# Kernel optimization log

Measured on AMD Instinct MI355X. Metric: run time of the kernel, lower is better.

## Reference

```python
import jax, jax.numpy as jnp
import numpy as np

HEADS = 4
DIM_HEAD = 32
SCALE = DIM_HEAD ** -0.5
EPS = 1e-5


def setup_inputs() -> dict:
    key = jax.random.key(0)
    ks = jax.random.split(key, 4)
    B, C, H, W = 16, 128, 32, 32
    hid = HEADS * DIM_HEAD  # 128
    return {
        "x": jax.random.normal(ks[0], (B, C, H, W), jnp.float32),
        "gn_weight": jnp.ones((C,), jnp.float32),
        "gn_bias": jnp.zeros((C,), jnp.float32),
        "w_qkv": jax.random.normal(ks[1], (3 * hid, C), jnp.float32) * 0.05,  # 1x1 conv, no bias
        "w_out": jax.random.normal(ks[2], (C, hid), jnp.float32) * 0.05,      # 1x1 conv
        "b_out": jax.random.normal(ks[3], (C,), jnp.float32) * 0.05,
    }


def reference(x, gn_weight, gn_bias, w_qkv, w_out, b_out):
    B, C, H, W = x.shape
    N = H * W
    # GroupNorm(num_groups=1): normalize over (C, H, W) per sample, per-channel affine
    mu = x.mean(axis=(1, 2, 3), keepdims=True)
    var = x.var(axis=(1, 2, 3), keepdims=True)
    xn = (x - mu) * jax.lax.rsqrt(var + EPS)
    xn = xn * gn_weight[None, :, None, None] + gn_bias[None, :, None, None]

    xf = xn.reshape(B, C, N)  # b c n
    qkv = jnp.einsum('bcn,oc->bon', xf, w_qkv)  # 1x1 conv == matmul over channels
    q, k, v = jnp.split(qkv, 3, axis=1)

    def to_heads(t):  # 'b (h c) x y -> b h (x y) c'
        return t.reshape(B, HEADS, DIM_HEAD, N).transpose(0, 1, 3, 2)  # b h n c

    q, k, v = map(to_heads, (q, k, v))

    q = jax.nn.softmax(q, axis=-2) * SCALE  # softmax over spatial tokens
    k = jax.nn.softmax(k, axis=-1)          # softmax over channel dim

    # Faithful to source einsums: contract over CHANNEL dim -> (b, h, N, N) context
    context = jnp.einsum('bhdc,bhec->bhde', k, v)      # b h n n
    out = jnp.einsum('bhde,bhdc->bhec', context, q)    # b h n c

    # 'b h (x y) c -> b (h c) x y'
    outf = out.transpose(0, 1, 3, 2).reshape(B, HEADS * DIM_HEAD, N)
    y = jnp.einsum('bcn,oc->bon', outf, w_out) + b_out[None, :, None]
    return y.reshape(B, C, H, W)
```

## Files before the change

### kernel.cpp

```cpp
#include <hip/hip_runtime.h>
#include <math.h>

#define CIN 128
#define NTOK 1024
#define SCALE_Q 0.17677669529663687f
#define GN_EPS 1e-5f
#define PB (CIN * NTOK)

#define WS_WQKVB 0
#define WS_WVT   16384
#define WS_PSTATS 24576
#define WS_PQSUM 25088
#define WS_PMT   57856
#define WS_WEFF  1106432
#define WS_BIAS  1237504

typedef __bf16 bf16x8 __attribute__((ext_vector_type(8)));
typedef float f32x4 __attribute__((ext_vector_type(4)));

__device__ __forceinline__ unsigned short f2bf(float f) {
    union { float f; unsigned u; } v; v.f = f;
    unsigned r = v.u + 0x7fffu + ((v.u >> 16) & 1u);
    return (unsigned short)(r >> 16);
}
__device__ __forceinline__ unsigned pack2(float a, float b) {
    return (unsigned)f2bf(a) | ((unsigned)f2bf(b) << 16);
}

__global__ __launch_bounds__(256) void k_pre(const float* __restrict__ x,
                                             const float* __restrict__ wqkv,
                                             float* __restrict__ ws) {
    float* pstats = ws + WS_PSTATS;
    unsigned short* wqkvb = (unsigned short*)(ws + WS_WQKVB);
    unsigned short* wvT = (unsigned short*)(ws + WS_WVT);
    __shared__ float sD[8];
    int bid = blockIdx.x, t = threadIdx.x;
    int lane = t & 63, wave = t >> 6;
    const float4* p = (const float4*)(x + (size_t)bid * 8192);
    float s = 0.f, s2 = 0.f;
    #pragma unroll
    for (int i = 0; i < 8; i++) {
        float4 v = p[t + 256 * i];
        s += v.x + v.y + v.z + v.w;
        s2 += v.x * v.x + v.y * v.y + v.z * v.z + v.w * v.w;
    }
    #pragma unroll
    for (int off = 32; off; off >>= 1) {
        s += __shfl_down(s, off);
        s2 += __shfl_down(s2, off);
    }
    if (lane == 0) { sD[wave * 2] = s; sD[wave * 2 + 1] = s2; }
    if (bid < 32) {
        float4 v = ((const float4*)(wqkv + bid * 1024))[t];
        uint2 pk2; pk2.x = pack2(v.x, v.y); pk2.y = pack2(v.z, v.w);
        *(uint2*)(wqkvb + bid * 1024 + t * 4) = pk2;
    } else if (bid < 48) {
        int g = bid - 32;
        int kk = g * 8 + (t >> 5), cq = t & 31;
        float v0 = wqkv[(256 + cq * 4 + 0) * 128 + kk];
        float v1 = wqkv[(256 + cq * 4 + 1) * 128 + kk];
        float v2 = wqkv[(256 + cq * 4 + 2) * 128 + kk];
        float v3 = wqkv[(256 + cq * 4 + 3) * 128 + kk];
        uint2 pk2; pk2.x = pack2(v0, v1); pk2.y = pack2(v2, v3);
        *(uint2*)(wvT + kk * 128 + cq * 4) = pk2;
    }
    __syncthreads();
    if (t == 0) {
        pstats[bid * 2] = sD[0] + sD[2] + sD[4] + sD[6];
        pstats[bid * 2 + 1] = sD[1] + sD[3] + sD[5] + sD[7];
    }
}

__global__ __launch_bounds__(512, 1) void k_qk(const float* __restrict__ x,
                                               const float* __restrict__ gw,
                                               const float* __restrict__ gb,
                                               float* __restrict__ ws) {
    __shared__ __align__(16) char smem[122880];
    unsigned short (*Al)[136] = (unsigned short(*)[136])smem;
    float (*Xl)[68] = (float(*)[68])(smem + 17408);
    unsigned short (*kTl)[68] = (unsigned short(*)[68])(smem + 17408);
    unsigned short (*qTl)[68] = (unsigned short(*)[68])(smem + 34816);
    unsigned short (*Bl)[136] = (unsigned short(*)[136])(smem + 52224);
    float* sD = (float*)(smem + 121856);

    unsigned short* wqkvb = (unsigned short*)(ws + WS_WQKVB);
    float* pstats = ws + WS_PSTATS;
    float* pqsum = ws + WS_PQSUM;
    float* pMT = ws + WS_PMT;

    int bid = blockIdx.x, t = threadIdx.x;
    int b = bid >> 4, nt = bid & 15;
    int lane = t & 63, wave = t >> 6;
    int l15 = lane & 15, lk = (lane >> 4) * 8;
    int sel = wave >> 1;
    int wn0 = (wave & 1) * 32;

    if (t < 32) sD[t] = pstats[b * 32 + t];
    int cx = t >> 2, qtr = t & 3;
    const float4* xsrc = (const float4*)(x + ((size_t)b * CIN + cx) * NTOK + nt * 64 + qtr * 16);
    float4 xr0 = xsrc[0], xr1 = xsrc[1], xr2 = xsrc[2], xr3 = xsrc[3];
    {
        int row = t >> 1, hf = t & 1;
        const uint4* src = (const uint4*)(wqkvb + (size_t)row * CIN + hf * 64);
        uint4* dst = (uint4*)&Bl[row][hf * 64];
        #pragma unroll
        for (int j = 0; j < 8; j++) dst[j] = src[j];
    }
    __syncthreads();
    float mu, rsv;
    {
        float s = 0.f, s2 = 0.f;
        #pragma unroll
        for (int i = 0; i < 16; i++) { s += sD[2 * i]; s2 += sD[2 * i + 1]; }
        mu = s * (1.f / PB);
        float var = s2 * (1.f / PB) - mu * mu;
        rsv = rsqrtf(var + GN_EPS);
    }
    {
        float g = gw[cx] * rsv, bb = gb[cx] - mu * g;
        float4 r0 = { xr0.x * g + bb, xr0.y * g + bb, xr0.z * g + bb, xr0.w * g + bb };
        float4 r1 = { xr1.x * g + bb, xr1.y * g + bb, xr1.z * g + bb, xr1.w * g + bb };
        float4 r2 = { xr2.x * g + bb, xr2.y * g + bb, xr2.z * g + bb, xr2.w * g + bb };
        float4 r3 = { xr3.x * g + bb, xr3.y * g + bb, xr3.z * g + bb, xr3.w * g + bb };
        *(float4*)&Xl[cx][qtr * 16 + 0] = r0;
        *(float4*)&Xl[cx][qtr * 16 + 4] = r1;
        *(float4*)&Xl[cx][qtr * 16 + 8] = r2;
        *(float4*)&Xl[cx][qtr * 16 + 12] = r3;
    }
    __syncthreads();
    {
        int n = t & 63, kq = (t >> 6) * 16;
        unsigned pk[8];
        #pragma unroll
        for (int j = 0; j < 8; j++) pk[j] = pack2(Xl[kq + 2 * j][n], Xl[kq + 2 * j + 1][n]);
        *(uint4*)&Al[n][kq] = *(uint4*)pk;
        *(uint4*)(&Al[n][kq] + 8) = *(uint4*)(pk + 4);
    }
    __syncthreads();
    f32x4 acc[2][4] = {};
    #pragma unroll
    for (int ks = 0; ks < 4; ks++) {
        bf16x8 av[2], bv[4];
        #pragma unroll
        for (int i = 0; i < 2; i++) av[i] = *(const bf16x8*)&Al[wn0 + i * 16 + l15][ks * 32 + lk];
        #pragma unroll
        for (int j = 0; j < 4; j++) bv[j] = *(const bf16x8*)&Bl[sel * 64 + j * 16 + l15][ks * 32 + lk];
        #pragma unroll
        for (int i = 0; i < 2; i++)
            #pragma unroll
            for (int j = 0; j < 4; j++)
                acc[i][j] = __builtin_amdgcn_mfma_f32_16x16x32_bf16(av[i], bv[j], acc[i][j], 0, 0, 0);
    }
    float e[2][4][4];
    #pragma unroll
    for (int i = 0; i < 2; i++)
        #pragma unroll
        for (int j = 0; j < 4; j++)
            #pragma unroll
            for (int r = 0; r < 4; r++) e[i][j][r] = __expf(acc[i][j][r]);

    if (sel >= 2) {
        #pragma unroll
        for (int i = 0; i < 2; i++)
            #pragma unroll
            for (int r = 0; r < 4; r++) {
                float e01 = e[i][0][r] + e[i][1][r];
                float e23 = e[i][2][r] + e[i][3][r];
                #pragma unroll
                for (int m = 1; m < 16; m <<= 1) {
                    e01 += __shfl_xor(e01, m);
                    e23 += __shfl_xor(e23, m);
                }
                float i01 = 1.f / e01, i23 = 1.f / e23;
                e[i][0][r] *= i01; e[i][1][r] *= i01;
                e[i][2][r] *= i23; e[i][3][r] *= i23;
            }
        #pragma unroll
        for (int i = 0; i < 2; i++)
            #pragma unroll
            for (int j = 0; j < 4; j++) {
                int ch = (sel - 2) * 64 + j * 16 + l15;
                int tokb = wn0 + i * 16 + (lane >> 4) * 4;
                *(unsigned*)&kTl[ch][tokb] = pack2(e[i][j][0], e[i][j][1]);
                *(unsigned*)&kTl[ch][tokb + 2] = pack2(e[i][j][2], e[i][j][3]);
            }
    } else {
        #pragma unroll
        for (int i = 0; i < 2; i++)
            #pragma unroll
            for (int j = 0; j < 4; j++) {
                int ch = sel * 64 + j * 16 + l15;
                int tokb = wn0 + i * 16 + (lane >> 4) * 4;
                *(unsigned*)&qTl[ch][tokb] = pack2(e[i][j][0], e[i][j][1]);
                *(unsigned*)&qTl[ch][tokb + 2] = pack2(e[i][j][2], e[i][j][3]);
            }
        #pragma unroll
        for (int j = 0; j < 4; j++) {
            float sq = 0.f;
            #pragma unroll
            for (int i = 0; i < 2; i++)
                #pragma unroll
                for (int r = 0; r < 4; r++) sq += e[i][j][r];
            sq += __shfl_xor(sq, 16);
            sq += __shfl_xor(sq, 32);
            if (lane < 16) sD[(wave & 1) * 128 + sel * 64 + j * 16 + lane] = sq;
        }
    }
    __syncthreads();
    if (t < 128) pqsum[(size_t)bid * 128 + t] = sD[t] + sD[128 + t];
    if (wave < 4) {
        int h = wave;
        f32x4 mac[2][2] = {};
        #pragma unroll
        for (int ks = 0; ks < 2; ks++) {
            bf16x8 av[2], bv[2];
            #pragma unroll
            for (int i = 0; i < 2; i++) av[i] = *(const bf16x8*)&qTl[h * 32 + i * 16 + l15][ks * 32 + lk];
            #pragma unroll
            for (int j = 0; j < 2; j++) bv[j] = *(const bf16x8*)&kTl[h * 32 + j * 16 + l15][ks * 32 + lk];
            #pragma unroll
            for (int i = 0; i < 2; i++)
                #pragma unroll
                for (int j = 0; j < 2; j++)
                    mac[i][j] = __builtin_amdgcn_mfma_f32_16x16x32_bf16(av[i], bv[j], mac[i][j], 0, 0, 0);
        }
        float* pmb = pMT + ((size_t)bid * 4 + h) * 1024;
        #pragma unroll
        for (int i = 0; i < 2; i++)
            #pragma unroll
            for (int j = 0; j < 2; j++)
                #pragma unroll
                for (int r = 0; r < 4; r++)
                    pmb[(i * 16 + (lane >> 4) * 4 + r) * 32 + j * 16 + l15] = mac[i][j][r];
    }
}

__global__ __launch_bounds__(512, 1) void k_weff(const float* __restrict__ gw,
                                                 const float* __restrict__ gb,
                                                 const float* __restrict__ wout,
                                                 const float* __restrict__ bout,
                                                 float* __restrict__ ws) {
    __shared__ __align__(16) char smem[116736];
    unsigned short (*pMTb)[32][40] = (unsigned short(*)[32][40])smem;
    unsigned short (*wvTb)[136] = (unsigned short(*)[136])(smem + 10240);
    unsigned short (*WeffL)[136] = (unsigned short(*)[136])(smem + 10240);
    unsigned short (*woutb)[136] = (unsigned short(*)[136])(smem + 45056);
    unsigned short (*B2T)[136] = (unsigned short(*)[136])(smem + 79872);
    float* sD = (float*)(smem + 114688);

    float* pstats = ws + WS_PSTATS;
    float* pqsum = ws + WS_PQSUM;
    float* pMT = ws + WS_PMT;
    unsigned short* wvT = (unsigned short*)(ws + WS_WVT);
    unsigned short* weffg = (unsigned short*)(ws + WS_WEFF);
    float* biasg = ws + WS_BIAS;

    int b = blockIdx.x, t = threadIdx.x;
    int lane = t & 63, wave = t >> 6;
    int l15 = lane & 15, lk = (lane >> 4) * 8;

    if (t < 32) sD[384 + t] = pstats[b * 32 + t];
    if (t < 128) {
        float s = 0.f;
        #pragma unroll
        for (int i = 0; i < 16; i++) s += pqsum[(size_t)(b * 16 + i) * 128 + t];
        sD[t] = SCALE_Q / s;
    }
    #pragma unroll
    for (int s2 = 0; s2 < 2; s2++) {
        int f4 = t * 2 + s2;
        int h = f4 >> 8, c = (f4 >> 3) & 31, cp0 = (f4 & 7) * 4;
        float4 m = { 0.f, 0.f, 0.f, 0.f };
        for (int i = 0; i < 16; i++) {
            float4 v = *(const float4*)&pMT[(((size_t)(b * 16 + i)) * 4 + h) * 1024 + c * 32 + cp0];
            m.x += v.x; m.y += v.y; m.z += v.z; m.w += v.w;
        }
        uint2 u; u.x = pack2(m.x, m.y); u.y = pack2(m.z, m.w);
        *(uint2*)&pMTb[h][c][cp0] = u;
    }
    {
        int row = t >> 2, q4 = t & 3;
        const uint4* src = (const uint4*)(wvT + row * 128) + q4 * 4;
        #pragma unroll
        for (int m = 0; m < 4; m++) *(uint4*)&wvTb[row][q4 * 32 + m * 8] = src[m];
    }
    {
        int row = t >> 2, q4 = t & 3;
        const float4* src = (const float4*)(wout + row * 128 + q4 * 32);
        #pragma unroll
        for (int i = 0; i < 8; i++) {
            float4 v = src[i];
            uint2 u; u.x = pack2(v.x, v.y); u.y = pack2(v.z, v.w);
            *(uint2*)&woutb[row][q4 * 32 + i * 4] = u;
        }
    }
    __syncthreads();
    if (t < 128) {
        float s = 0.f, s2 = 0.f;
        #pragma unroll
        for (int i = 0; i < 16; i++) { s += sD[384 + 2 * i]; s2 += sD[384 + 2 * i + 1]; }
        float mu = s * (1.f / PB);
        float var = s2 * (1.f / PB) - mu * mu;
        float rs = rsqrtf(var + GN_EPS);
        float gsc = gw[t] * rs;
        sD[128 + t] = gsc;
        sD[256 + t] = gb[t] - mu * gsc;
    }
    __syncthreads();
    {
        int h = wave >> 1, kh = wave & 1;
        f32x4 mac[2][4] = {};
        bf16x8 av[2];
        #pragma unroll
        for (int i = 0; i < 2; i++) av[i] = *(const bf16x8*)&pMTb[h][i * 16 + l15][lk];
        #pragma unroll
        for (int j = 0; j < 4; j++) {
            bf16x8 bv = *(const bf16x8*)&wvTb[kh * 64 + j * 16 + l15][h * 32 + lk];
            #pragma unroll
            for (int i = 0; i < 2; i++)
                mac[i][j] = __builtin_amdgcn_mfma_f32_16x16x32_bf16(av[i], bv, mac[i][j], 0, 0, 0);
        }
        #pragma unroll
        for (int i = 0; i < 2; i++)
            #pragma unroll
            for (int j = 0; j < 4; j++) {
                int k = kh * 64 + j * 16 + l15;
                int cb = h * 32 + i * 16 + (lane >> 4) * 4;
                float q0 = sD[cb], q1 = sD[cb + 1], q2 = sD[cb + 2], q3 = sD[cb + 3];
                uint2 u;
                u.x = pack2(mac[i][j][0] * q0, mac[i][j][1] * q1);
                u.y = pack2(mac[i][j][2] * q2, mac[i][j][3] * q3);
                *(uint2*)&B2T[k][cb] = u;
            }
    }
    __syncthreads();
    {
        f32x4 acc[8] = {};
        #pragma unroll
        for (int ks = 0; ks < 4; ks++) {
            bf16x8 av = *(const bf16x8*)&woutb[wave * 16 + l15][ks * 32 + lk];
            #pragma unroll
            for (int j = 0; j < 8; j++) {
                bf16x8 bv = *(const bf16x8*)&B2T[j * 16 + l15][ks * 32 + lk];
                acc[j] = __builtin_amdgcn_mfma_f32_16x16x32_bf16(av, bv, acc[j], 0, 0, 0);
            }
        }
        float gs[8], bbv[8];
        #pragma unroll
        for (int j = 0; j < 8; j++) {
            int k = j * 16 + l15;
            gs[j] = sD[128 + k];
            bbv[j] = sD[256 + k];
        }
        #pragma unroll
        for (int r = 0; r < 4; r++) {
            int o = wave * 16 + (lane >> 4) * 4 + r;
            float pb = 0.f;
            #pragma unroll
            for (int j = 0; j < 8; j++) {
                float wv = acc[j][r];
                pb += wv * bbv[j];
                WeffL[o][j * 16 + l15] = f2bf(wv * gs[j]);
            }
            pb += __shfl_xor(pb, 1);
            pb += __shfl_xor(pb, 2);
            pb += __shfl_xor(pb, 4);
            pb += __shfl_xor(pb, 8);
            if (l15 == 0) biasg[b * 128 + o] = bout[o] + pb;
        }
    }
    __syncthreads();
    {
        int row = t >> 2, q4 = t & 3;
        #pragma unroll
        for (int m = 0; m < 4; m++)
            *(uint4*)(weffg + (size_t)b * 16384 + row * 128 + q4 * 32 + m * 8) =
                *(uint4*)&WeffL[row][q4 * 32 + m * 8];
    }
}

__global__ __launch_bounds__(512, 1) void k_out2(const float* __restrict__ x,
                                                 float* __restrict__ ws,
                                                 float* __restrict__ y) {
    __shared__ __align__(16) char smem[87552];
    unsigned short (*Wfb)[136] = (unsigned short(*)[136])smem;
    float (*Xl)[68] = (float(*)[68])(smem + 34816);
    unsigned short (*xT)[136] = (unsigned short(*)[136])(smem + 69632);
    float* sDb = (float*)(smem + 87040);

    unsigned short* weffg = (unsigned short*)(ws + WS_WEFF);
    float* biasg = ws + WS_BIAS;

    int nt = blockIdx.x, b = blockIdx.y, t = threadIdx.x;
    int lane = t & 63, wave = t >> 6;
    int l15 = lane & 15, lk = (lane >> 4) * 8;

    if (t < 128) sDb[t] = biasg[b * 128 + t];
    {
        int row = t >> 2, q4 = t & 3;
        const uint4* src = (const uint4*)(weffg + (size_t)b * 16384 + row * 128) + q4 * 4;
        #pragma unroll
        for (int m = 0; m < 4; m++) *(uint4*)&Wfb[row][q4 * 32 + m * 8] = src[m];
    }
    {
        int cx = t >> 2, qtr = t & 3;
        const float4* xsrc = (const float4*)(x + ((size_t)b * CIN + cx) * NTOK + nt * 64 + qtr * 16);
        #pragma unroll
        for (int i = 0; i < 4; i++) *(float4*)&Xl[cx][qtr * 16 + i * 4] = xsrc[i];
    }
    __syncthreads();
    {
        int n = t & 63, kq = (t >> 6) * 16;
        unsigned pk[8];
        #pragma unroll
        for (int j = 0; j < 8; j++) pk[j] = pack2(Xl[kq + 2 * j][n], Xl[kq + 2 * j + 1][n]);
        *(uint4*)&xT[n][kq] = *(uint4*)pk;
        *(uint4*)(&xT[n][kq] + 8) = *(uint4*)(pk + 4);
    }
    __syncthreads();
    int o0 = (wave >> 1) * 32, n0 = (wave & 1) * 32;
    f32x4 acc[2][2] = {};
    #pragma unroll
    for (int ks = 0; ks < 4; ks++) {
        bf16x8 av[2], bv[2];
        #pragma unroll
        for (int i = 0; i < 2; i++) av[i] = *(const bf16x8*)&Wfb[o0 + i * 16 + l15][ks * 32 + lk];
        #pragma unroll
        for (int j = 0; j < 2; j++) bv[j] = *(const bf16x8*)&xT[n0 + j * 16 + l15][ks * 32 + lk];
        #pragma unroll
        for (int i = 0; i < 2; i++)
            #pragma unroll
            for (int j = 0; j < 2; j++)
                acc[i][j] = __builtin_amdgcn_mfma_f32_16x16x32_bf16(av[i], bv[j], acc[i][j], 0, 0, 0);
    }
    #pragma unroll
    for (int i = 0; i < 2; i++)
        #pragma unroll
        for (int r = 0; r < 4; r++) {
            int o = o0 + i * 16 + (lane >> 4) * 4 + r;
            float bias = sDb[o];
            float* yp = y + ((size_t)b * CIN + o) * NTOK + nt * 64 + n0;
            #pragma unroll
            for (int j = 0; j < 2; j++) yp[j * 16 + l15] = acc[i][j][r] + bias;
        }
}

extern "C" void kernel_launch(void* const* d_in, const int* in_sizes, int n_in,
                              void* d_out, int out_size, void* d_ws, size_t ws_size,
                              hipStream_t stream) {
    const float* x = (const float*)d_in[0];
    const float* gw = (const float*)d_in[1];
    const float* gb = (const float*)d_in[2];
    const float* wqkv = (const float*)d_in[3];
    const float* wout = (const float*)d_in[4];
    const float* bout = (const float*)d_in[5];
    float* y = (float*)d_out;
    float* ws = (float*)d_ws;

    k_pre<<<dim3(256), 256, 0, stream>>>(x, wqkv, ws);
    k_qk<<<dim3(256), 512, 0, stream>>>(x, gw, gb, ws);
    k_weff<<<dim3(16), 512, 0, stream>>>(gw, gb, wout, bout, ws);
    k_out2<<<dim3(16, 16), 512, 0, stream>>>(x, ws, y);
}
```

Baseline: 97.63 us.

## Fuse Weff fold into output kernel and reduce partials with atomics

```diff
diff --git a/kernel.cpp b/kernel.cpp
--- a/kernel.cpp
+++ b/kernel.cpp
@@ -10,10 +10,8 @@
 #define WS_WQKVB 0
 #define WS_WVT   16384
 #define WS_PSTATS 24576
-#define WS_PQSUM 25088
-#define WS_PMT   57856
-#define WS_WEFF  1106432
-#define WS_BIAS  1237504
+#define WS_QSUMG 25088
+#define WS_MG    27136
 
 typedef __bf16 bf16x8 __attribute__((ext_vector_type(8)));
 typedef float f32x4 __attribute__((ext_vector_type(4)));
@@ -36,6 +34,8 @@
     __shared__ float sD[8];
     int bid = blockIdx.x, t = threadIdx.x;
     int lane = t & 63, wave = t >> 6;
+    int gid = bid * 256 + t;
+    if (gid < 18432) ws[WS_QSUMG + gid] = 0.f;
     const float4* p = (const float4*)(x + (size_t)bid * 8192);
     float s = 0.f, s2 = 0.f;
     #pragma unroll
@@ -75,30 +75,35 @@
                                                const float* __restrict__ gw,
                                                const float* __restrict__ gb,
                                                float* __restrict__ ws) {
-    __shared__ __align__(16) char smem[122880];
+    __shared__ __align__(16) char smem[121856];
     unsigned short (*Al)[136] = (unsigned short(*)[136])smem;
-    float (*Xl)[68] = (float(*)[68])(smem + 17408);
-    unsigned short (*kTl)[68] = (unsigned short(*)[68])(smem + 17408);
-    unsigned short (*qTl)[68] = (unsigned short(*)[68])(smem + 34816);
-    unsigned short (*Bl)[136] = (unsigned short(*)[136])(smem + 52224);
-    float* sD = (float*)(smem + 121856);
+    unsigned short (*Bl)[136] = (unsigned short(*)[136])(smem + 17408);
+    unsigned short (*kTl)[68] = (unsigned short(*)[68])(smem + 87040);
+    unsigned short (*qTl)[68] = (unsigned short(*)[68])(smem + 104448);
 
     unsigned short* wqkvb = (unsigned short*)(ws + WS_WQKVB);
     float* pstats = ws + WS_PSTATS;
-    float* pqsum = ws + WS_PQSUM;
-    float* pMT = ws + WS_PMT;
+    float* qsumg = ws + WS_QSUMG;
+    float* Mg = ws + WS_MG;
 
     int bid = blockIdx.x, t = threadIdx.x;
     int b = bid >> 4, nt = bid & 15;
     int lane = t & 63, wave = t >> 6;
     int l15 = lane & 15, lk = (lane >> 4) * 8;
-    int sel = wave >> 1;
-    int wn0 = (wave & 1) * 32;
-
-    if (t < 32) sD[t] = pstats[b * 32 + t];
-    int cx = t >> 2, qtr = t & 3;
-    const float4* xsrc = (const float4*)(x + ((size_t)b * CIN + cx) * NTOK + nt * 64 + qtr * 16);
-    float4 xr0 = xsrc[0], xr1 = xsrc[1], xr2 = xsrc[2], xr3 = xsrc[3];
+    int sel = wave >> 1, wn0 = (wave & 1) * 32;
+
+    float mu, rsv;
+    {
+        float s = 0.f, s2 = 0.f;
+        #pragma unroll
+        for (int i = 0; i < 16; i++) {
+            s += pstats[b * 32 + 2 * i];
+            s2 += pstats[b * 32 + 2 * i + 1];
+        }
+        mu = s * (1.f / PB);
+        float var = s2 * (1.f / PB) - mu * mu;
+        rsv = rsqrtf(var + GN_EPS);
+    }
     {
         int row = t >> 1, hf = t & 1;
         const uint4* src = (const uint4*)(wqkvb + (size_t)row * CIN + hf * 64);
@@ -106,35 +111,19 @@
         #pragma unroll
         for (int j = 0; j < 8; j++) dst[j] = src[j];
     }
-    __syncthreads();
-    float mu, rsv;
-    {
-        float s = 0.f, s2 = 0.f;
-        #pragma unroll
-        for (int i = 0; i < 16; i++) { s += sD[2 * i]; s2 += sD[2 * i + 1]; }
-        mu = s * (1.f / PB);
-        float var = s2 * (1.f / PB) - mu * mu;
-        rsv = rsqrtf(var + GN_EPS);
-    }
-    {
-        float g = gw[cx] * rsv, bb = gb[cx] - mu * g;
-        float4 r0 = { xr0.x * g + bb, xr0.y * g + bb, xr0.z * g + bb, xr0.w * g + bb };
-        float4 r1 = { xr1.x * g + bb, xr1.y * g + bb, xr1.z * g + bb, xr1.w * g + bb };
-        float4 r2 = { xr2.x * g + bb, xr2.y * g + bb, xr2.z * g + bb, xr2.w * g + bb };
-        float4 r3 = { xr3.x * g + bb, xr3.y * g + bb, xr3.z * g + bb, xr3.w * g + bb };
-        *(float4*)&Xl[cx][qtr * 16 + 0] = r0;
-        *(float4*)&Xl[cx][qtr * 16 + 4] = r1;
-        *(float4*)&Xl[cx][qtr * 16 + 8] = r2;
-        *(float4*)&Xl[cx][qtr * 16 + 12] = r3;
-    }
-    __syncthreads();
-    {
-        int n = t & 63, kq = (t >> 6) * 16;
-        unsigned pk[8];
-        #pragma unroll
-        for (int j = 0; j < 8; j++) pk[j] = pack2(Xl[kq + 2 * j][n], Xl[kq + 2 * j + 1][n]);
-        *(uint4*)&Al[n][kq] = *(uint4*)pk;
-        *(uint4*)(&Al[n][kq] + 8) = *(uint4*)(pk + 4);
+    {
+        int c = t & 127, seg = t >> 7;
+        const float4* xsrc = (const float4*)(x + ((size_t)b * CIN + c) * NTOK + nt * 64 + seg * 16);
+        float g = gw[c] * rsv, bb = gb[c] - mu * g;
+        #pragma unroll
+        for (int q4 = 0; q4 < 4; q4++) {
+            float4 v = xsrc[q4];
+            int n = seg * 16 + q4 * 4;
+            Al[n + 0][c] = f2bf(v.x * g + bb);
+            Al[n + 1][c] = f2bf(v.y * g + bb);
+            Al[n + 2][c] = f2bf(v.z * g + bb);
+            Al[n + 3][c] = f2bf(v.w * g + bb);
+        }
     }
     __syncthreads();
     f32x4 acc[2][4] = {};
@@ -203,11 +192,10 @@
                 for (int r = 0; r < 4; r++) sq += e[i][j][r];
             sq += __shfl_xor(sq, 16);
             sq += __shfl_xor(sq, 32);
-            if (lane < 16) sD[(wave & 1) * 128 + sel * 64 + j * 16 + lane] = sq;
-        }
-    }
-    __syncthreads();
-    if (t < 128) pqsum[(size_t)bid * 128 + t] = sD[t] + sD[128 + t];
+            if (lane < 16) atomicAdd(&qsumg[b * 128 + sel * 64 + j * 16 + lane], sq);
+        }
+    }
+    __syncthreads();
     if (wave < 4) {
         int h = wave;
         f32x4 mac[2][2] = {};
@@ -224,63 +212,82 @@
                 for (int j = 0; j < 2; j++)
                     mac[i][j] = __builtin_amdgcn_mfma_f32_16x16x32_bf16(av[i], bv[j], mac[i][j], 0, 0, 0);
         }
-        float* pmb = pMT + ((size_t)bid * 4 + h) * 1024;
+        float* mb = Mg + (size_t)b * 4096 + h * 1024;
         #pragma unroll
         for (int i = 0; i < 2; i++)
             #pragma unroll
             for (int j = 0; j < 2; j++)
                 #pragma unroll
                 for (int r = 0; r < 4; r++)
-                    pmb[(i * 16 + (lane >> 4) * 4 + r) * 32 + j * 16 + l15] = mac[i][j][r];
-    }
-}
-
-__global__ __launch_bounds__(512, 1) void k_weff(const float* __restrict__ gw,
-                                                 const float* __restrict__ gb,
-                                                 const float* __restrict__ wout,
-                                                 const float* __restrict__ bout,
-                                                 float* __restrict__ ws) {
-    __shared__ __align__(16) char smem[116736];
-    unsigned short (*pMTb)[32][40] = (unsigned short(*)[32][40])smem;
-    unsigned short (*wvTb)[136] = (unsigned short(*)[136])(smem + 10240);
-    unsigned short (*WeffL)[136] = (unsigned short(*)[136])(smem + 10240);
-    unsigned short (*woutb)[136] = (unsigned short(*)[136])(smem + 45056);
-    unsigned short (*B2T)[136] = (unsigned short(*)[136])(smem + 79872);
-    float* sD = (float*)(smem + 114688);
+                    atomicAdd(&mb[(i * 16 + (lane >> 4) * 4 + r) * 32 + j * 16 + l15], mac[i][j][r]);
+    }
+}
+
+__global__ __launch_bounds__(512, 1) void k_fold_out(const float* __restrict__ x,
+                                                     const float* __restrict__ gw,
+                                                     const float* __restrict__ gb,
+                                                     const float* __restrict__ wout,
+                                                     const float* __restrict__ bout,
+                                                     float* __restrict__ ws,
+                                                     float* __restrict__ y) {
+    __shared__ __align__(16) char smem[132608];
+    unsigned short (*Al)[136] = (unsigned short(*)[136])smem;
+    unsigned short (*pMTb)[32][40] = (unsigned short(*)[32][40])(smem + 17408);
+    unsigned short (*wvTb)[136] = (unsigned short(*)[136])(smem + 27648);
+    unsigned short (*WeffL)[136] = (unsigned short(*)[136])(smem + 27648);
+    unsigned short (*woutb)[136] = (unsigned short(*)[136])(smem + 62464);
+    unsigned short (*B2T)[136] = (unsigned short(*)[136])(smem + 97280);
+    float* biasL = (float*)(smem + 132096);
 
     float* pstats = ws + WS_PSTATS;
-    float* pqsum = ws + WS_PQSUM;
-    float* pMT = ws + WS_PMT;
-    unsigned short* wvT = (unsigned short*)(ws + WS_WVT);
-    unsigned short* weffg = (unsigned short*)(ws + WS_WEFF);
-    float* biasg = ws + WS_BIAS;
-
-    int b = blockIdx.x, t = threadIdx.x;
+    float* qsumg = ws + WS_QSUMG;
+    float* Mg = ws + WS_MG;
+    unsigned short* wvTg = (unsigned short*)(ws + WS_WVT);
+
+    int bid = blockIdx.x, t = threadIdx.x;
+    int b = bid >> 4, nt = bid & 15;
     int lane = t & 63, wave = t >> 6;
     int l15 = lane & 15, lk = (lane >> 4) * 8;
 
-    if (t < 32) sD[384 + t] = pstats[b * 32 + t];
-    if (t < 128) {
-        float s = 0.f;
-        #pragma unroll
-        for (int i = 0; i < 16; i++) s += pqsum[(size_t)(b * 16 + i) * 128 + t];
-        sD[t] = SCALE_Q / s;
-    }
-    #pragma unroll
-    for (int s2 = 0; s2 < 2; s2++) {
-        int f4 = t * 2 + s2;
-        int h = f4 >> 8, c = (f4 >> 3) & 31, cp0 = (f4 & 7) * 4;
-        float4 m = { 0.f, 0.f, 0.f, 0.f };
+    float mu, rsv;
+    {
+        float s = 0.f, s2 = 0.f;
+        #pragma unroll
         for (int i = 0; i < 16; i++) {
-            float4 v = *(const float4*)&pMT[(((size_t)(b * 16 + i)) * 4 + h) * 1024 + c * 32 + cp0];
-            m.x += v.x; m.y += v.y; m.z += v.z; m.w += v.w;
-        }
-        uint2 u; u.x = pack2(m.x, m.y); u.y = pack2(m.z, m.w);
-        *(uint2*)&pMTb[h][c][cp0] = u;
+            s += pstats[b * 32 + 2 * i];
+            s2 += pstats[b * 32 + 2 * i + 1];
+        }
+        mu = s * (1.f / PB);
+        float var = s2 * (1.f / PB) - mu * mu;
+        rsv = rsqrtf(var + GN_EPS);
+    }
+    {
+        int c = t & 127, seg = t >> 7;
+        const float4* xsrc = (const float4*)(x + ((size_t)b * CIN + c) * NTOK + nt * 64 + seg * 16);
+        float g = gw[c] * rsv, bb = gb[c] - mu * g;
+        #pragma unroll
+        for (int q4 = 0; q4 < 4; q4++) {
+            float4 v = xsrc[q4];
+            int n = seg * 16 + q4 * 4;
+            Al[n + 0][c] = f2bf(v.x * g + bb);
+            Al[n + 1][c] = f2bf(v.y * g + bb);
+            Al[n + 2][c] = f2bf(v.z * g + bb);
+            Al[n + 3][c] = f2bf(v.w * g + bb);
+        }
+    }
+    {
+        int base = t * 8;
+        int h = base >> 10, idx = base & 1023, c = idx >> 5, cp0 = idx & 31;
+        float4 m0 = *(const float4*)&Mg[(size_t)b * 4096 + base];
+        float4 m1 = *(const float4*)&Mg[(size_t)b * 4096 + base + 4];
+        uint4 u;
+        u.x = pack2(m0.x, m0.y); u.y = pack2(m0.z, m0.w);
+        u.z = pack2(m1.x, m1.y); u.w = pack2(m1.z, m1.w);
+        *(uint4*)&pMTb[h][c][cp0] = u;
     }
     {
         int row = t >> 2, q4 = t & 3;
-        const uint4* src = (const uint4*)(wvT + row * 128) + q4 * 4;
+        const uint4* src = (const uint4*)(wvTg + row * 128) + q4 * 4;
         #pragma unroll
         for (int m = 0; m < 4; m++) *(uint4*)&wvTb[row][q4 * 32 + m * 8] = src[m];
     }
@@ -294,18 +301,7 @@
             *(uint2*)&woutb[row][q4 * 32 + i * 4] = u;
         }
     }
-    __syncthreads();
-    if (t < 128) {
-        float s = 0.f, s2 = 0.f;
-        #pragma unroll
-        for (int i = 0; i < 16; i++) { s += sD[384 + 2 * i]; s2 += sD[384 + 2 * i + 1]; }
-        float mu = s * (1.f / PB);
-        float var = s2 * (1.f / PB) - mu * mu;
-        float rs = rsqrtf(var + GN_EPS);
-        float gsc = gw[t] * rs;
-        sD[128 + t] = gsc;
-        sD[256 + t] = gb[t] - mu * gsc;
-    }
+    if (t < 128) biasL[t] = bout[t];
     __syncthreads();
     {
         int h = wave >> 1, kh = wave & 1;
@@ -321,128 +317,68 @@
                 mac[i][j] = __builtin_amdgcn_mfma_f32_16x16x32_bf16(av[i], bv, mac[i][j], 0, 0, 0);
         }
         #pragma unroll
-        for (int i = 0; i < 2; i++)
+        for (int i = 0; i < 2; i++) {
+            int cb = h * 32 + i * 16 + (lane >> 4) * 4;
+            float4 qs = *(const float4*)&qsumg[b * 128 + cb];
+            float q0 = SCALE_Q / qs.x, q1 = SCALE_Q / qs.y;
+            float q2 = SCALE_Q / qs.z, q3 = SCALE_Q / qs.w;
             #pragma unroll
             for (int j = 0; j < 4; j++) {
                 int k = kh * 64 + j * 16 + l15;
-                int cb = h * 32 + i * 16 + (lane >> 4) * 4;
-                float q0 = sD[cb], q1 = sD[cb + 1], q2 = sD[cb + 2], q3 = sD[cb + 3];
                 uint2 u;
                 u.x = pack2(mac[i][j][0] * q0, mac[i][j][1] * q1);
                 u.y = pack2(mac[i][j][2] * q2, mac[i][j][3] * q3);
                 *(uint2*)&B2T[k][cb] = u;
             }
-    }
-    __syncthreads();
-    {
-        f32x4 acc[8] = {};
+        }
+    }
+    __syncthreads();
+    {
+        f32x4 a2[8] = {};
         #pragma unroll
         for (int ks = 0; ks < 4; ks++) {
             bf16x8 av = *(const bf16x8*)&woutb[wave * 16 + l15][ks * 32 + lk];
             #pragma unroll
             for (int j = 0; j < 8; j++) {
                 bf16x8 bv = *(const bf16x8*)&B2T[j * 16 + l15][ks * 32 + lk];
-                acc[j] = __builtin_amdgcn_mfma_f32_16x16x32_bf16(av, bv, acc[j], 0, 0, 0);
-            }
-        }
-        float gs[8], bbv[8];
-        #pragma unroll
-        for (int j = 0; j < 8; j++) {
-            int k = j * 16 + l15;
-            gs[j] = sD[128 + k];
-            bbv[j] = sD[256 + k];
-        }
-        #pragma unroll
-        for (int r = 0; r < 4; r++) {
-            int o = wave * 16 + (lane >> 4) * 4 + r;
-            float pb = 0.f;
-            #pragma unroll
-            for (int j = 0; j < 8; j++) {
-                float wv = acc[j][r];
-                pb += wv * bbv[j];
-                WeffL[o][j * 16 + l15] = f2bf(wv * gs[j]);
-            }
-            pb += __shfl_xor(pb, 1);
-            pb += __shfl_xor(pb, 2);
-            pb += __shfl_xor(pb, 4);
-            pb += __shfl_xor(pb, 8);
-            if (l15 == 0) biasg[b * 128 + o] = bout[o] + pb;
-        }
-    }
-    __syncthreads();
-    {
-        int row = t >> 2, q4 = t & 3;
-        #pragma unroll
-        for (int m = 0; m < 4; m++)
-            *(uint4*)(weffg + (size_t)b * 16384 + row * 128 + q4 * 32 + m * 8) =
-                *(uint4*)&WeffL[row][q4 * 32 + m * 8];
-    }
-}
-
-__global__ __launch_bounds__(512, 1) void k_out2(const float* __restrict__ x,
-                                                 float* __restrict__ ws,
-                                                 float* __restrict__ y) {
-    __shared__ __align__(16) char smem[87552];
-    unsigned short (*Wfb)[136] = (unsigned short(*)[136])smem;
-    float (*Xl)[68] = (float(*)[68])(smem + 34816);
-    unsigned short (*xT)[136] = (unsigned short(*)[136])(smem + 69632);
-    float* sDb = (float*)(smem + 87040);
-
-    unsigned short* weffg = (unsigned short*)(ws + WS_WEFF);
-    float* biasg = ws + WS_BIAS;
-
-    int nt = blockIdx.x, b = blockIdx.y, t = threadIdx.x;
-    int lane = t & 63, wave = t >> 6;
-    int l15 = lane & 15, lk = (lane >> 4) * 8;
-
-    if (t < 128) sDb[t] = biasg[b * 128 + t];
-    {
-        int row = t >> 2, q4 = t & 3;
-        const uint4* src = (const uint4*)(weffg + (size_t)b * 16384 + row * 128) + q4 * 4;
-        #pragma unroll
-        for (int m = 0; m < 4; m++) *(uint4*)&Wfb[row][q4 * 32 + m * 8] = src[m];
-    }
-    {
-        int cx = t >> 2, qtr = t & 3;
-        const float4* xsrc = (const float4*)(x + ((size_t)b * CIN + cx) * NTOK + nt * 64 + qtr * 16);
-        #pragma unroll
-        for (int i = 0; i < 4; i++) *(float4*)&Xl[cx][qtr * 16 + i * 4] = xsrc[i];
-    }
-    __syncthreads();
-    {
-        int n = t & 63, kq = (t >> 6) * 16;
-        unsigned pk[8];
-        #pragma unroll
-        for (int j = 0; j < 8; j++) pk[j] = pack2(Xl[kq + 2 * j][n], Xl[kq + 2 * j + 1][n]);
-        *(uint4*)&xT[n][kq] = *(uint4*)pk;
-        *(uint4*)(&xT[n][kq] + 8) = *(uint4*)(pk + 4);
-    }
-    __syncthreads();
-    int o0 = (wave >> 1) * 32, n0 = (wave & 1) * 32;
-    f32x4 acc[2][2] = {};
-    #pragma unroll
-    for (int ks = 0; ks < 4; ks++) {
-        bf16x8 av[2], bv[2];
-        #pragma unroll
-        for (int i = 0; i < 2; i++) av[i] = *(const bf16x8*)&Wfb[o0 + i * 16 + l15][ks * 32 + lk];
-        #pragma unroll
-        for (int j = 0; j < 2; j++) bv[j] = *(const bf16x8*)&xT[n0 + j * 16 + l15][ks * 32 + lk];
-        #pragma unroll
-        for (int i = 0; i < 2; i++)
-            #pragma unroll
-            for (int j = 0; j < 2; j++)
-                acc[i][j] = __builtin_amdgcn_mfma_f32_16x16x32_bf16(av[i], bv[j], acc[i][j], 0, 0, 0);
-    }
-    #pragma unroll
-    for (int i = 0; i < 2; i++)
-        #pragma unroll
-        for (int r = 0; r < 4; r++) {
-            int o = o0 + i * 16 + (lane >> 4) * 4 + r;
-            float bias = sDb[o];
-            float* yp = y + ((size_t)b * CIN + o) * NTOK + nt * 64 + n0;
-            #pragma unroll
-            for (int j = 0; j < 2; j++) yp[j * 16 + l15] = acc[i][j][r] + bias;
-        }
+                a2[j] = __builtin_amdgcn_mfma_f32_16x16x32_bf16(av, bv, a2[j], 0, 0, 0);
+            }
+        }
+        __syncthreads();
+        #pragma unroll
+        for (int j = 0; j < 8; j++)
+            #pragma unroll
+            for (int r = 0; r < 4; r++)
+                WeffL[wave * 16 + (lane >> 4) * 4 + r][j * 16 + l15] = f2bf(a2[j][r]);
+    }
+    __syncthreads();
+    {
+        int o0 = (wave >> 1) * 32, n0 = (wave & 1) * 32;
+        f32x4 ya[2][2] = {};
+        #pragma unroll
+        for (int ks = 0; ks < 4; ks++) {
+            bf16x8 av[2], bv[2];
+            #pragma unroll
+            for (int i = 0; i < 2; i++) av[i] = *(const bf16x8*)&WeffL[o0 + i * 16 + l15][ks * 32 + lk];
+            #pragma unroll
+            for (int j = 0; j < 2; j++) bv[j] = *(const bf16x8*)&Al[n0 + j * 16 + l15][ks * 32 + lk];
+            #pragma unroll
+            for (int i = 0; i < 2; i++)
+                #pragma unroll
+                for (int j = 0; j < 2; j++)
+                    ya[i][j] = __builtin_amdgcn_mfma_f32_16x16x32_bf16(av[i], bv[j], ya[i][j], 0, 0, 0);
+        }
+        #pragma unroll
+        for (int i = 0; i < 2; i++)
+            #pragma unroll
+            for (int r = 0; r < 4; r++) {
+                int o = o0 + i * 16 + (lane >> 4) * 4 + r;
+                float bias = biasL[o];
+                float* yp = y + ((size_t)b * CIN + o) * NTOK + nt * 64 + n0;
+                #pragma unroll
+                for (int j = 0; j < 2; j++) yp[j * 16 + l15] = ya[i][j][r] + bias;
+            }
+    }
 }
 
 extern "C" void kernel_launch(void* const* d_in, const int* in_sizes, int n_in,
@@ -459,6 +395,5 @@
 
     k_pre<<<dim3(256), 256, 0, stream>>>(x, wqkv, ws);
     k_qk<<<dim3(256), 512, 0, stream>>>(x, gw, gb, ws);
-    k_weff<<<dim3(16), 512, 0, stream>>>(gw, gb, wout, bout, ws);
-    k_out2<<<dim3(16, 16), 512, 0, stream>>>(x, ws, y);
-}
+    k_fold_out<<<dim3(256), 512, 0, stream>>>(x, gw, gb, wout, bout, ws, y);
+}
```

Measured after the change: 92.09 us. -5.7%, faster.
